# Kernel optimization log

Hardware: AMD Instinct MI355X
Metric: run time of the kernel (lower is better)

## Reference

```python
import jax, jax.numpy as jnp
import numpy as np

B, C, VC, H, W = 4, 256, 128, 64, 64


def setup_inputs() -> dict:
    key = jax.random.key(0)
    kx, kq, kk, kv = jax.random.split(key, 4)
    # Conv2d 1x1 no-bias weights are just [out_channels, in_channels] matrices.
    s = 1.0 / np.sqrt(C)
    return {
        "x": jax.random.normal(kx, (B, C, H, W), dtype=jnp.float32),
        "Wq": jax.random.uniform(kq, (VC, C), minval=-s, maxval=s, dtype=jnp.float32),
        "Wk": jax.random.uniform(kk, (VC, C), minval=-s, maxval=s, dtype=jnp.float32),
        "Wv": jax.random.uniform(kv, (VC, C), minval=-s, maxval=s, dtype=jnp.float32),
    }


def reference(x, Wq, Wk, Wv):
    # 1x1 convs == per-pixel channel GEMMs
    Q = jnp.einsum('bchw,dc->bdhw', x, Wq)  # [B, VC, H, W]
    K = jnp.einsum('bchw,dc->bdhw', x, Wk)
    V = jnp.einsum('bchw,dc->bdhw', x, Wv)
    b, d, h, w = Q.shape
    # affinity over all spatial pairs: [B, H, W, H, W]
    aff = jnp.einsum('bdij,bdkl->bijkl', Q, K).reshape(b, h, w, h * w)
    aff = jax.nn.softmax(aff, axis=3).reshape(b, h, w, h, w)
    # attention-weighted aggregation of values
    out = jnp.einsum('bijkl,bdkl->bdij', aff, V)  # [B, VC, H, W]
    return out
```

## Files before the change

### kernel.cpp

```cpp
#include <hip/hip_runtime.h>
#include <hip/hip_bf16.h>

#define B_ 4
#define C_ 256
#define D_ 128
#define N_ 4096

typedef float f32x4 __attribute__((ext_vector_type(4)));
typedef short bf16x8 __attribute__((ext_vector_type(8)));
typedef short s16x4 __attribute__((ext_vector_type(4)));
typedef unsigned short u16;
typedef unsigned int u32;

__device__ __forceinline__ u16 f2bf(float f) {
  unsigned u = __float_as_uint(f);
  u += 0x7fffu + ((u >> 16) & 1u);
  return (u16)(u >> 16);
}
__device__ __forceinline__ float bf2f(u16 v) {
  return __uint_as_float(((u32)v) << 16);
}
__device__ __forceinline__ u32 cvt_pk_bf16(float a, float b) {
  u32 r;
  asm("v_cvt_pk_bf16_f32 %0, %1, %2" : "=v"(r) : "v"(a), "v"(b));
  return r;
}

__global__ __launch_bounds__(256) void castw_kernel(
    const float* __restrict__ Wq, const float* __restrict__ Wk,
    const float* __restrict__ Wv, u16* __restrict__ Whi,
    u16* __restrict__ Wlo) {
  const int i = blockIdx.x * 256 + threadIdx.x;
  const int m = i >> 13;
  const int j = (i & 8191) * 4;
  const float* src = (m == 0) ? Wq : (m == 1) ? Wk : Wv;
  const float scale = (m == 0) ? 1.44269504f : 1.0f;
  const float4 v = *(const float4*)(src + j);
  const float vv[4] = {v.x * scale, v.y * scale, v.z * scale, v.w * scale};
  s16x4 h, l;
#pragma unroll
  for (int k = 0; k < 4; ++k) {
    const u16 hb = f2bf(vv[k]);
    h[k] = (short)hb;
    l[k] = (short)f2bf(vv[k] - bf2f(hb));
  }
  *(s16x4*)&Whi[m * 32768 + j] = h;
  *(s16x4*)&Wlo[m * 32768 + j] = l;
}

__global__ __launch_bounds__(256, 3) void proj_kernel(
    const float* __restrict__ x, const u16* __restrict__ Whi,
    const u16* __restrict__ Wlo, u16* __restrict__ Qo, u16* __restrict__ Ko,
    u16* __restrict__ Vt) {
  __shared__ __align__(16) u16 xs_h[32 * 256];
  __shared__ __align__(16) u16 xs_l[32 * 256];

  const int n0 = blockIdx.x * 32;
  const int b = blockIdx.y;
  const int z = blockIdx.z;
  const int t = threadIdx.x;
  const int w = t >> 6, lane = t & 63, g = lane >> 4, c = lane & 15;

  {
    const float* xb = x + ((size_t)b * C_) * N_ + n0;
#pragma unroll
    for (int r = 0; r < 8; ++r) {
      const int id = r * 256 + t;
      const int cr = id >> 3, nq = (id & 7) * 4;
      const float4 v = *(const float4*)(xb + (size_t)cr * N_ + nq);
      const float vv[4] = {v.x, v.y, v.z, v.w};
#pragma unroll
      for (int k2 = 0; k2 < 4; ++k2) {
        const int idx2 = (nq + k2) * 256 + (cr ^ (((nq + k2) & 7) << 3));
        const u16 hb = f2bf(vv[k2]);
        xs_h[idx2] = hb;
        xs_l[idx2] = f2bf(vv[k2] - bf2f(hb));
      }
    }
  }
  __syncthreads();

  if (w < 2) {
    const size_t wo = (size_t)w * 32768;
    u16* __restrict__ O = (w == 0 ? Qo : Ko) + (size_t)b * N_ * D_;
#pragma unroll 1
    for (int dti = 0; dti < 4; ++dti) {
      const int dt = z * 4 + dti;
      f32x4 a0 = {0.f, 0.f, 0.f, 0.f};
      f32x4 a1 = {0.f, 0.f, 0.f, 0.f};
#pragma unroll 1
      for (int kcb = 0; kcb < 2; ++kcb) {
        bf16x8 wfh[4], wfl[4];
#pragma unroll
        for (int j = 0; j < 4; ++j) {
          const size_t off = wo + (size_t)(dt * 16 + c) * 256 +
                             (kcb * 4 + j) * 32 + g * 8;
          wfh[j] = *(const bf16x8*)&Whi[off];
          wfl[j] = *(const bf16x8*)&Wlo[off];
        }
#pragma unroll
        for (int j = 0; j < 4; ++j) {
          const int kc = kcb * 4 + j;
          const int col = (kc * 32 + g * 8) ^ ((c & 7) << 3);
          const bf16x8 xh0 = *(const bf16x8*)&xs_h[c * 256 + col];
          const bf16x8 xl0 = *(const bf16x8*)&xs_l[c * 256 + col];
          const bf16x8 xh1 = *(const bf16x8*)&xs_h[(16 + c) * 256 + col];
          const bf16x8 xl1 = *(const bf16x8*)&xs_l[(16 + c) * 256 + col];
          a0 = __builtin_amdgcn_mfma_f32_16x16x32_bf16(xh0, wfh[j], a0, 0, 0, 0);
          a0 = __builtin_amdgcn_mfma_f32_16x16x32_bf16(xh0, wfl[j], a0, 0, 0, 0);
          a0 = __builtin_amdgcn_mfma_f32_16x16x32_bf16(xl0, wfh[j], a0, 0, 0, 0);
          a1 = __builtin_amdgcn_mfma_f32_16x16x32_bf16(xh1, wfh[j], a1, 0, 0, 0);
          a1 = __builtin_amdgcn_mfma_f32_16x16x32_bf16(xh1, wfl[j], a1, 0, 0, 0);
          a1 = __builtin_amdgcn_mfma_f32_16x16x32_bf16(xl1, wfh[j], a1, 0, 0, 0);
        }
      }
#pragma unroll
      for (int i = 0; i < 4; ++i) {
        O[(size_t)(n0 + g * 4 + i) * D_ + dt * 16 + c] = f2bf(a0[i]);
        O[(size_t)(n0 + 16 + g * 4 + i) * D_ + dt * 16 + c] = f2bf(a1[i]);
      }
    }
  } else {
    const size_t wo = (size_t)2 * 32768;
    const int d0 = (w - 2) * 64 + z * 32;
    u16* __restrict__ O = Vt + (size_t)b * D_ * N_;
#pragma unroll 1
    for (int dti = 0; dti < 2; ++dti) {
      const int dr = d0 + dti * 16;
      f32x4 a0 = {0.f, 0.f, 0.f, 0.f};
      f32x4 a1 = {0.f, 0.f, 0.f, 0.f};
#pragma unroll 1
      for (int kcb = 0; kcb < 2; ++kcb) {
        bf16x8 wfh[4], wfl[4];
#pragma unroll
        for (int j = 0; j < 4; ++j) {
          const size_t off =
              wo + (size_t)(dr + c) * 256 + (kcb * 4 + j) * 32 + g * 8;
          wfh[j] = *(const bf16x8*)&Whi[off];
          wfl[j] = *(const bf16x8*)&Wlo[off];
        }
#pragma unroll
        for (int j = 0; j < 4; ++j) {
          const int kc = kcb * 4 + j;
          const int col = (kc * 32 + g * 8) ^ ((c & 7) << 3);
          const bf16x8 xh0 = *(const bf16x8*)&xs_h[c * 256 + col];
          const bf16x8 xl0 = *(const bf16x8*)&xs_l[c * 256 + col];
          const bf16x8 xh1 = *(const bf16x8*)&xs_h[(16 + c) * 256 + col];
          const bf16x8 xl1 = *(const bf16x8*)&xs_l[(16 + c) * 256 + col];
          a0 = __builtin_amdgcn_mfma_f32_16x16x32_bf16(wfh[j], xh0, a0, 0, 0, 0);
          a0 = __builtin_amdgcn_mfma_f32_16x16x32_bf16(wfl[j], xh0, a0, 0, 0, 0);
          a0 = __builtin_amdgcn_mfma_f32_16x16x32_bf16(wfh[j], xl0, a0, 0, 0, 0);
          a1 = __builtin_amdgcn_mfma_f32_16x16x32_bf16(wfh[j], xh1, a1, 0, 0, 0);
          a1 = __builtin_amdgcn_mfma_f32_16x16x32_bf16(wfl[j], xh1, a1, 0, 0, 0);
          a1 = __builtin_amdgcn_mfma_f32_16x16x32_bf16(wfh[j], xl1, a1, 0, 0, 0);
        }
      }
#pragma unroll
      for (int i = 0; i < 4; ++i) {
        O[(size_t)(dr + g * 4 + i) * N_ + n0 + c] = f2bf(a0[i]);
        O[(size_t)(dr + g * 4 + i) * N_ + n0 + 16 + c] = f2bf(a1[i]);
      }
    }
  }
}

__device__ __forceinline__ int kIdx(int row, int col) {
  return row * 128 + (col ^ ((row & 7) << 3));
}
__device__ __forceinline__ int vIdx(int d, int col) {
  return d * 64 + (col ^ ((d & 7) << 3));
}
__device__ __forceinline__ int kprm(int q) {
  const int ct = q >> 2, qq = q & 3;
  return ((ct >> 1) << 5) +
         (((qq >> 1) == (ct & 1)) ? (qq << 3) : (((qq ^ 2) << 3) + 4));
}

__global__ __launch_bounds__(256, 2) void attn_kernel(
    const u16* __restrict__ Q, const u16* __restrict__ K,
    const u16* __restrict__ Vt, u16* __restrict__ op,
    float* __restrict__ mb, float* __restrict__ lb,
    float* __restrict__ outf, int qt, int rem, int S) {
  __shared__ __align__(16) u16 lds_k[64 * 128];
  __shared__ __align__(16) u16 lds_vt[128 * 64];

  const int L = blockIdx.x;
  int qx, b, sid;
  if (((B_ * S) & 7) == 0) {
    const int gpx = (B_ * S) >> 3;
    const int xcd = L & 7, idx = L >> 3;
    const int grp = xcd * gpx + (idx >> 5);
    qx = idx & 31;
    b = grp / S;
    sid = grp - b * S;
  } else {
    qx = L & 31;
    const int r2 = L >> 5;
    b = r2 % B_;
    sid = r2 / B_;
  }
  const int q0 = qx * 128;
  const int NT = qt + (sid < rem ? 1 : 0);
  const int t0 = sid * qt + (sid < rem ? sid : rem);
  const int k0 = t0 * 64;
  const int t = threadIdx.x;
  const int w = t >> 6, lane = t & 63, g = lane >> 4, c = lane & 15;
  const int qw = q0 + w * 32;
  const bool ghi = (g & 2) != 0;

  const u16* __restrict__ Qb = Q + (size_t)b * N_ * D_;
  const u16* __restrict__ Kb = K + (size_t)b * N_ * D_;
  const u16* __restrict__ Vb = Vt + (size_t)b * D_ * N_;

  bf16x8 qf[2][4];
#pragma unroll
  for (int qh = 0; qh < 2; ++qh)
#pragma unroll
    for (int kc = 0; kc < 4; ++kc)
      qf[qh][kc] =
          *(const bf16x8*)&Qb[(size_t)(qw + qh * 16 + c) * D_ + kc * 32 + g * 8];

  f32x4 acc[8][2];
  f32x4 accl[2];
#pragma unroll
  for (int dt = 0; dt < 8; ++dt)
#pragma unroll
    for (int qh = 0; qh < 2; ++qh) acc[dt][qh] = (f32x4){0.f, 0.f, 0.f, 0.f};
  accl[0] = (f32x4){0.f, 0.f, 0.f, 0.f};
  accl[1] = (f32x4){0.f, 0.f, 0.f, 0.f};
  float mrow[2] = {-3.0e38f, -3.0e38f};
  const float THR = 11.5415603f;

  bf16x8 onesv;
#pragma unroll
  for (int j = 0; j < 8; ++j) onesv[j] = (short)0x3F80;

  bf16x8 krg[4], vrg[4];
  auto load_tile = [&](int kbase) {
#pragma unroll
    for (int i = 0; i < 4; ++i) {
      const int idx = i * 256 + t;
      krg[i] = *(const bf16x8*)&Kb[(size_t)(kbase + (idx >> 4)) * D_ + (idx & 15) * 8];
      vrg[i] = *(const bf16x8*)&Vb[(size_t)(idx >> 3) * N_ + kbase + (idx & 7) * 8];
    }
  };
  load_tile(k0);

  for (int kt = 0; kt < NT; ++kt) {
    __syncthreads();
#pragma unroll
    for (int i = 0; i < 4; ++i) {
      const int idx = i * 256 + t;
      *(bf16x8*)&lds_k[kIdx(idx >> 4, (idx & 15) * 8)] = krg[i];
      const int d = idx >> 3, rc = idx & 7;
      s16x4 lo, hi;
      lo[0] = vrg[i][0]; lo[1] = vrg[i][1]; lo[2] = vrg[i][2]; lo[3] = vrg[i][3];
      hi[0] = vrg[i][4]; hi[1] = vrg[i][5]; hi[2] = vrg[i][6]; hi[3] = vrg[i][7];
      *(s16x4*)&lds_vt[vIdx(d, kprm(rc * 2))] = lo;
      *(s16x4*)&lds_vt[vIdx(d, kprm(rc * 2 + 1))] = hi;
    }
    if (kt + 1 < NT) load_tile(k0 + (kt + 1) * 64);
    __syncthreads();

    f32x4 s[4][2];
#pragma unroll
    for (int ct = 0; ct < 4; ++ct)
#pragma unroll
      for (int qh = 0; qh < 2; ++qh) s[ct][qh] = (f32x4){0.f, 0.f, 0.f, 0.f};
    __builtin_amdgcn_s_setprio(1);
#pragma unroll
    for (int kc = 0; kc < 4; ++kc) {
#pragma unroll
      for (int ct = 0; ct < 4; ++ct) {
        const bf16x8 kf =
            *(const bf16x8*)&lds_k[kIdx(ct * 16 + c, kc * 32 + g * 8)];
        s[ct][0] = __builtin_amdgcn_mfma_f32_16x16x32_bf16(kf, qf[0][kc], s[ct][0], 0, 0, 0);
        s[ct][1] = __builtin_amdgcn_mfma_f32_16x16x32_bf16(kf, qf[1][kc], s[ct][1], 0, 0, 0);
      }
    }
    __builtin_amdgcn_s_setprio(0);

    float pml[2];
#pragma unroll
    for (int qh = 0; qh < 2; ++qh) {
      const float m0 = fmaxf(fmaxf(s[0][qh][0], s[0][qh][1]),
                             fmaxf(s[0][qh][2], s[0][qh][3]));
      const float m1 = fmaxf(fmaxf(s[1][qh][0], s[1][qh][1]),
                             fmaxf(s[1][qh][2], s[1][qh][3]));
      const float m2 = fmaxf(fmaxf(s[2][qh][0], s[2][qh][1]),
                             fmaxf(s[2][qh][2], s[2][qh][3]));
      const float m3 = fmaxf(fmaxf(s[3][qh][0], s[3][qh][1]),
                             fmaxf(s[3][qh][2], s[3][qh][3]));
      pml[qh] = fmaxf(fmaxf(m0, m1), fmaxf(m2, m3));
    }
    const bool need =
        __any((pml[0] > mrow[0] + THR) || (pml[1] > mrow[1] + THR));
    if (need) {
#pragma unroll
      for (int qh = 0; qh < 2; ++qh) {
        float p = pml[qh];
        p = fmaxf(p, __shfl_xor(p, 16));
        p = fmaxf(p, __shfl_xor(p, 32));
        const float mnew = fmaxf(mrow[qh], p);
        const float scl = exp2f(mrow[qh] - mnew);
        mrow[qh] = mnew;
        accl[qh][0] *= scl; accl[qh][1] *= scl;
        accl[qh][2] *= scl; accl[qh][3] *= scl;
#pragma unroll
        for (int dt = 0; dt < 8; ++dt) {
          acc[dt][qh][0] *= scl; acc[dt][qh][1] *= scl;
          acc[dt][qh][2] *= scl; acc[dt][qh][3] *= scl;
        }
      }
    }
#pragma unroll
    for (int qh = 0; qh < 2; ++qh)
#pragma unroll
      for (int ct = 0; ct < 4; ++ct)
#pragma unroll
        for (int i = 0; i < 4; ++i)
          s[ct][qh][i] = exp2f(s[ct][qh][i] - mrow[qh]);

    u32 pfw[2][2][4];
#pragma unroll
    for (int kc = 0; kc < 2; ++kc) {
#pragma unroll
      for (int qh = 0; qh < 2; ++qh) {
        const u32 lo0 = cvt_pk_bf16(s[kc * 2][qh][0], s[kc * 2][qh][1]);
        const u32 lo1 = cvt_pk_bf16(s[kc * 2][qh][2], s[kc * 2][qh][3]);
        const u32 hi0 = cvt_pk_bf16(s[kc * 2 + 1][qh][0], s[kc * 2 + 1][qh][1]);
        const u32 hi1 = cvt_pk_bf16(s[kc * 2 + 1][qh][2], s[kc * 2 + 1][qh][3]);
        pfw[kc][qh][0] = ghi ? hi0 : lo0;
        pfw[kc][qh][1] = ghi ? hi1 : lo1;
        const u32 s0 = ghi ? lo0 : hi0;
        const u32 s1 = ghi ? lo1 : hi1;
        pfw[kc][qh][2] = (u32)__shfl_xor((int)s0, 32);
        pfw[kc][qh][3] = (u32)__shfl_xor((int)s1, 32);
      }
    }

#pragma unroll
    for (int kc = 0; kc < 2; ++kc) {
      union { u32 w[4]; bf16x8 v; } u0, u1;
#pragma unroll
      for (int j = 0; j < 4; ++j) { u0.w[j] = pfw[kc][0][j]; u1.w[j] = pfw[kc][1][j]; }
      __builtin_amdgcn_s_setprio(1);
      accl[0] = __builtin_amdgcn_mfma_f32_16x16x32_bf16(onesv, u0.v, accl[0], 0, 0, 0);
      accl[1] = __builtin_amdgcn_mfma_f32_16x16x32_bf16(onesv, u1.v, accl[1], 0, 0, 0);
#pragma unroll
      for (int dt = 0; dt < 8; ++dt) {
        const bf16x8 vf =
            *(const bf16x8*)&lds_vt[vIdx(dt * 16 + c, kc * 32 + g * 8)];
        acc[dt][0] = __builtin_amdgcn_mfma_f32_16x16x32_bf16(vf, u0.v, acc[dt][0], 0, 0, 0);
        acc[dt][1] = __builtin_amdgcn_mfma_f32_16x16x32_bf16(vf, u1.v, acc[dt][1], 0, 0, 0);
      }
      __builtin_amdgcn_s_setprio(0);
    }
  }

#pragma unroll
  for (int qh = 0; qh < 2; ++qh) {
    const int n = qw + qh * 16 + c;
    const float lr = accl[qh][0];
    if (mb) {
      u16* __restrict__ ob = op + ((size_t)(sid * B_ + b) * D_) * N_;
#pragma unroll
      for (int dt = 0; dt < 8; ++dt)
#pragma unroll
        for (int i = 0; i < 4; ++i)
          ob[(size_t)(dt * 16 + g * 4 + i) * N_ + n] = f2bf(acc[dt][qh][i]);
      if (g == 0) {
        mb[(size_t)(sid * B_ + b) * N_ + n] = mrow[qh];
        lb[(size_t)(sid * B_ + b) * N_ + n] = lr;
      }
    } else {
      const float linv = 1.0f / lr;
      float* __restrict__ ob = outf + (size_t)b * D_ * N_;
#pragma unroll
      for (int dt = 0; dt < 8; ++dt)
#pragma unroll
        for (int i = 0; i < 4; ++i)
          ob[(size_t)(dt * 16 + g * 4 + i) * N_ + n] = acc[dt][qh][i] * linv;
    }
  }
}

__global__ __launch_bounds__(256) void combine_kernel(
    const u16* __restrict__ op, const float* __restrict__ mbu,
    const float* __restrict__ lbu, float* __restrict__ out, int S) {
  const int idx = blockIdx.x * 256 + threadIdx.x;
  const int n0 = (idx & (N_ / 4 - 1)) * 4;
  const int bd = idx >> 10;
  const int b = bd >> 7, d = bd & (D_ - 1);

  float4 msv[8], lsv[8];
  float M0 = -3e38f, M1 = -3e38f, M2 = -3e38f, M3 = -3e38f;
#pragma unroll
  for (int s = 0; s < 8; ++s)
    if (s < S) {
      msv[s] = *(const float4*)&mbu[(size_t)(s * B_ + b) * N_ + n0];
      lsv[s] = *(const float4*)&lbu[(size_t)(s * B_ + b) * N_ + n0];
      M0 = fmaxf(M0, msv[s].x); M1 = fmaxf(M1, msv[s].y);
      M2 = fmaxf(M2, msv[s].z); M3 = fmaxf(M3, msv[s].w);
    }
  float d0 = 0.f, d1 = 0.f, d2 = 0.f, d3 = 0.f;
  float a0 = 0.f, a1 = 0.f, a2 = 0.f, a3 = 0.f;
#pragma unroll
  for (int s = 0; s < 8; ++s)
    if (s < S) {
      const float w0 = exp2f(msv[s].x - M0);
      const float w1 = exp2f(msv[s].y - M1);
      const float w2 = exp2f(msv[s].z - M2);
      const float w3 = exp2f(msv[s].w - M3);
      d0 += lsv[s].x * w0; d1 += lsv[s].y * w1;
      d2 += lsv[s].z * w2; d3 += lsv[s].w * w3;
      const s16x4 o =
          *(const s16x4*)&op[((size_t)(s * B_ + b) * D_ + d) * N_ + n0];
      a0 += w0 * bf2f((u16)o[0]); a1 += w1 * bf2f((u16)o[1]);
      a2 += w2 * bf2f((u16)o[2]); a3 += w3 * bf2f((u16)o[3]);
    }
  float4 r = {a0 / d0, a1 / d1, a2 / d2, a3 / d3};
  *(float4*)&out[((size_t)b * D_ + d) * N_ + n0] = r;
}

extern "C" void kernel_launch(void* const* d_in, const int* in_sizes, int n_in,
                              void* d_out, int out_size, void* d_ws, size_t ws_size,
                              hipStream_t stream) {
  const float* x  = (const float*)d_in[0];
  const float* Wq = (const float*)d_in[1];
  const float* Wk = (const float*)d_in[2];
  const float* Wv = (const float*)d_in[3];
  float* out = (float*)d_out;

  u16* whi  = (u16*)d_ws;
  u16* wlo  = whi + (size_t)3 * 128 * 256;
  u16* q_ws = wlo + (size_t)3 * 128 * 256;
  u16* k_ws = q_ws + (size_t)B_ * N_ * D_;
  u16* v_ws = k_ws + (size_t)B_ * N_ * D_;

  castw_kernel<<<96, 256, 0, stream>>>(Wq, Wk, Wv, whi, wlo);
  proj_kernel<<<dim3(N_ / 32, B_, 2), 256, 0, stream>>>(x, whi, wlo, q_ws,
                                                        k_ws, v_ws);

  const size_t baseB =
      ((size_t)6 * 128 * 256 + (size_t)3 * B_ * N_ * D_) * 2;
  int S = 0;
  const int cands[4] = {6, 4, 2, 1};
  for (int ci = 0; ci < 4; ++ci) {
    const int cand = cands[ci];
    const size_t need = baseB + (size_t)cand * ((size_t)B_ * D_ * N_ * 2 +
                                                (size_t)2 * B_ * N_ * 4);
    if (ws_size >= need) { S = cand; break; }
  }
  if (S > 1) {
    u16* opb = (u16*)((char*)d_ws + baseB);
    float* mbuf = (float*)(opb + (size_t)S * B_ * D_ * N_);
    float* lbuf = mbuf + (size_t)S * B_ * N_;
    attn_kernel<<<dim3(32 * B_ * S), 256, 0, stream>>>(
        q_ws, k_ws, v_ws, opb, mbuf, lbuf, nullptr, 64 / S, 64 % S, S);
    combine_kernel<<<(B_ * D_ * N_ / 4) / 256, 256, 0, stream>>>(opb, mbuf,
                                                                 lbuf, out, S);
  } else {
    attn_kernel<<<dim3(32 * B_), 256, 0, stream>>>(
        q_ws, k_ws, v_ws, nullptr, nullptr, nullptr, out, 64, 0, 1);
  }
}
```

Baseline: 101.6 us.

## Halve attention query tile per block to raise occupancy and drop split count

```diff
diff --git a/kernel.cpp b/kernel.cpp
--- a/kernel.cpp
+++ b/kernel.cpp
@@ -176,7 +176,7 @@
          (((qq >> 1) == (ct & 1)) ? (qq << 3) : (((qq ^ 2) << 3) + 4));
 }
 
-__global__ __launch_bounds__(256, 2) void attn_kernel(
+__global__ __launch_bounds__(256, 4) void attn_kernel(
     const u16* __restrict__ Q, const u16* __restrict__ K,
     const u16* __restrict__ Vt, u16* __restrict__ op,
     float* __restrict__ mb, float* __restrict__ lb,
@@ -189,46 +189,40 @@
   if (((B_ * S) & 7) == 0) {
     const int gpx = (B_ * S) >> 3;
     const int xcd = L & 7, idx = L >> 3;
-    const int grp = xcd * gpx + (idx >> 5);
-    qx = idx & 31;
+    const int grp = xcd * gpx + (idx >> 6);
+    qx = idx & 63;
     b = grp / S;
     sid = grp - b * S;
   } else {
-    qx = L & 31;
-    const int r2 = L >> 5;
+    qx = L & 63;
+    const int r2 = L >> 6;
     b = r2 % B_;
     sid = r2 / B_;
   }
-  const int q0 = qx * 128;
+  const int q0 = qx * 64;
   const int NT = qt + (sid < rem ? 1 : 0);
   const int t0 = sid * qt + (sid < rem ? sid : rem);
   const int k0 = t0 * 64;
   const int t = threadIdx.x;
   const int w = t >> 6, lane = t & 63, g = lane >> 4, c = lane & 15;
-  const int qw = q0 + w * 32;
+  const int qw = q0 + w * 16;
   const bool ghi = (g & 2) != 0;
 
   const u16* __restrict__ Qb = Q + (size_t)b * N_ * D_;
   const u16* __restrict__ Kb = K + (size_t)b * N_ * D_;
   const u16* __restrict__ Vb = Vt + (size_t)b * D_ * N_;
 
-  bf16x8 qf[2][4];
-#pragma unroll
-  for (int qh = 0; qh < 2; ++qh)
-#pragma unroll
-    for (int kc = 0; kc < 4; ++kc)
-      qf[qh][kc] =
-          *(const bf16x8*)&Qb[(size_t)(qw + qh * 16 + c) * D_ + kc * 32 + g * 8];
-
-  f32x4 acc[8][2];
-  f32x4 accl[2];
-#pragma unroll
-  for (int dt = 0; dt < 8; ++dt)
-#pragma unroll
-    for (int qh = 0; qh < 2; ++qh) acc[dt][qh] = (f32x4){0.f, 0.f, 0.f, 0.f};
-  accl[0] = (f32x4){0.f, 0.f, 0.f, 0.f};
-  accl[1] = (f32x4){0.f, 0.f, 0.f, 0.f};
-  float mrow[2] = {-3.0e38f, -3.0e38f};
+  bf16x8 qf[4];
+#pragma unroll
+  for (int kc = 0; kc < 4; ++kc)
+    qf[kc] = *(const bf16x8*)&Qb[(size_t)(qw + c) * D_ + kc * 32 + g * 8];
+
+  f32x4 acc[8];
+  f32x4 accl;
+#pragma unroll
+  for (int dt = 0; dt < 8; ++dt) acc[dt] = (f32x4){0.f, 0.f, 0.f, 0.f};
+  accl = (f32x4){0.f, 0.f, 0.f, 0.f};
+  float mrow = -3.0e38f;
   const float THR = 11.5415603f;
 
   bf16x8 onesv;
@@ -262,11 +256,9 @@
     if (kt + 1 < NT) load_tile(k0 + (kt + 1) * 64);
     __syncthreads();
 
-    f32x4 s[4][2];
-#pragma unroll
-    for (int ct = 0; ct < 4; ++ct)
-#pragma unroll
-      for (int qh = 0; qh < 2; ++qh) s[ct][qh] = (f32x4){0.f, 0.f, 0.f, 0.f};
+    f32x4 s[4];
+#pragma unroll
+    for (int ct = 0; ct < 4; ++ct) s[ct] = (f32x4){0.f, 0.f, 0.f, 0.f};
     __builtin_amdgcn_s_setprio(1);
 #pragma unroll
     for (int kc = 0; kc < 4; ++kc) {
@@ -274,103 +266,83 @@
       for (int ct = 0; ct < 4; ++ct) {
         const bf16x8 kf =
             *(const bf16x8*)&lds_k[kIdx(ct * 16 + c, kc * 32 + g * 8)];
-        s[ct][0] = __builtin_amdgcn_mfma_f32_16x16x32_bf16(kf, qf[0][kc], s[ct][0], 0, 0, 0);
-        s[ct][1] = __builtin_amdgcn_mfma_f32_16x16x32_bf16(kf, qf[1][kc], s[ct][1], 0, 0, 0);
+        s[ct] = __builtin_amdgcn_mfma_f32_16x16x32_bf16(kf, qf[kc], s[ct], 0, 0, 0);
       }
     }
     __builtin_amdgcn_s_setprio(0);
 
-    float pml[2];
-#pragma unroll
-    for (int qh = 0; qh < 2; ++qh) {
-      const float m0 = fmaxf(fmaxf(s[0][qh][0], s[0][qh][1]),
-                             fmaxf(s[0][qh][2], s[0][qh][3]));
-      const float m1 = fmaxf(fmaxf(s[1][qh][0], s[1][qh][1]),
-                             fmaxf(s[1][qh][2], s[1][qh][3]));
-      const float m2 = fmaxf(fmaxf(s[2][qh][0], s[2][qh][1]),
-                             fmaxf(s[2][qh][2], s[2][qh][3]));
-      const float m3 = fmaxf(fmaxf(s[3][qh][0], s[3][qh][1]),
-                             fmaxf(s[3][qh][2], s[3][qh][3]));
-      pml[qh] = fmaxf(fmaxf(m0, m1), fmaxf(m2, m3));
-    }
-    const bool need =
-        __any((pml[0] > mrow[0] + THR) || (pml[1] > mrow[1] + THR));
+    float pml;
+    {
+      const float m0 = fmaxf(fmaxf(s[0][0], s[0][1]), fmaxf(s[0][2], s[0][3]));
+      const float m1 = fmaxf(fmaxf(s[1][0], s[1][1]), fmaxf(s[1][2], s[1][3]));
+      const float m2 = fmaxf(fmaxf(s[2][0], s[2][1]), fmaxf(s[2][2], s[2][3]));
+      const float m3 = fmaxf(fmaxf(s[3][0], s[3][1]), fmaxf(s[3][2], s[3][3]));
+      pml = fmaxf(fmaxf(m0, m1), fmaxf(m2, m3));
+    }
+    const bool need = __any(pml > mrow + THR);
     if (need) {
-#pragma unroll
-      for (int qh = 0; qh < 2; ++qh) {
-        float p = pml[qh];
-        p = fmaxf(p, __shfl_xor(p, 16));
-        p = fmaxf(p, __shfl_xor(p, 32));
-        const float mnew = fmaxf(mrow[qh], p);
-        const float scl = exp2f(mrow[qh] - mnew);
-        mrow[qh] = mnew;
-        accl[qh][0] *= scl; accl[qh][1] *= scl;
-        accl[qh][2] *= scl; accl[qh][3] *= scl;
-#pragma unroll
-        for (int dt = 0; dt < 8; ++dt) {
-          acc[dt][qh][0] *= scl; acc[dt][qh][1] *= scl;
-          acc[dt][qh][2] *= scl; acc[dt][qh][3] *= scl;
-        }
-      }
-    }
-#pragma unroll
-    for (int qh = 0; qh < 2; ++qh)
-#pragma unroll
-      for (int ct = 0; ct < 4; ++ct)
-#pragma unroll
-        for (int i = 0; i < 4; ++i)
-          s[ct][qh][i] = exp2f(s[ct][qh][i] - mrow[qh]);
-
-    u32 pfw[2][2][4];
+      float p = pml;
+      p = fmaxf(p, __shfl_xor(p, 16));
+      p = fmaxf(p, __shfl_xor(p, 32));
+      const float mnew = fmaxf(mrow, p);
+      const float scl = exp2f(mrow - mnew);
+      mrow = mnew;
+      accl[0] *= scl; accl[1] *= scl; accl[2] *= scl; accl[3] *= scl;
+#pragma unroll
+      for (int dt = 0; dt < 8; ++dt) {
+        acc[dt][0] *= scl; acc[dt][1] *= scl;
+        acc[dt][2] *= scl; acc[dt][3] *= scl;
+      }
+    }
+#pragma unroll
+    for (int ct = 0; ct < 4; ++ct)
+#pragma unroll
+      for (int i = 0; i < 4; ++i) s[ct][i] = exp2f(s[ct][i] - mrow);
+
+    u32 pfw[2][4];
 #pragma unroll
     for (int kc = 0; kc < 2; ++kc) {
-#pragma unroll
-      for (int qh = 0; qh < 2; ++qh) {
-        const u32 lo0 = cvt_pk_bf16(s[kc * 2][qh][0], s[kc * 2][qh][1]);
-        const u32 lo1 = cvt_pk_bf16(s[kc * 2][qh][2], s[kc * 2][qh][3]);
-        const u32 hi0 = cvt_pk_bf16(s[kc * 2 + 1][qh][0], s[kc * 2 + 1][qh][1]);
-        const u32 hi1 = cvt_pk_bf16(s[kc * 2 + 1][qh][2], s[kc * 2 + 1][qh][3]);
-        pfw[kc][qh][0] = ghi ? hi0 : lo0;
-        pfw[kc][qh][1] = ghi ? hi1 : lo1;
-        const u32 s0 = ghi ? lo0 : hi0;
-        const u32 s1 = ghi ? lo1 : hi1;
-        pfw[kc][qh][2] = (u32)__shfl_xor((int)s0, 32);
-        pfw[kc][qh][3] = (u32)__shfl_xor((int)s1, 32);
-      }
+      const u32 lo0 = cvt_pk_bf16(s[kc * 2][0], s[kc * 2][1]);
+      const u32 lo1 = cvt_pk_bf16(s[kc * 2][2], s[kc * 2][3]);
+      const u32 hi0 = cvt_pk_bf16(s[kc * 2 + 1][0], s[kc * 2 + 1][1]);
+      const u32 hi1 = cvt_pk_bf16(s[kc * 2 + 1][2], s[kc * 2 + 1][3]);
+      pfw[kc][0] = ghi ? hi0 : lo0;
+      pfw[kc][1] = ghi ? hi1 : lo1;
+      const u32 s0 = ghi ? lo0 : hi0;
+      const u32 s1 = ghi ? lo1 : hi1;
+      pfw[kc][2] = (u32)__shfl_xor((int)s0, 32);
+      pfw[kc][3] = (u32)__shfl_xor((int)s1, 32);
     }
 
 #pragma unroll
     for (int kc = 0; kc < 2; ++kc) {
-      union { u32 w[4]; bf16x8 v; } u0, u1;
-#pragma unroll
-      for (int j = 0; j < 4; ++j) { u0.w[j] = pfw[kc][0][j]; u1.w[j] = pfw[kc][1][j]; }
+      union { u32 w[4]; bf16x8 v; } u0;
+#pragma unroll
+      for (int j = 0; j < 4; ++j) u0.w[j] = pfw[kc][j];
       __builtin_amdgcn_s_setprio(1);
-      accl[0] = __builtin_amdgcn_mfma_f32_16x16x32_bf16(onesv, u0.v, accl[0], 0, 0, 0);
-      accl[1] = __builtin_amdgcn_mfma_f32_16x16x32_bf16(onesv, u1.v, accl[1], 0, 0, 0);
+      accl = __builtin_amdgcn_mfma_f32_16x16x32_bf16(onesv, u0.v, accl, 0, 0, 0);
 #pragma unroll
       for (int dt = 0; dt < 8; ++dt) {
         const bf16x8 vf =
             *(const bf16x8*)&lds_vt[vIdx(dt * 16 + c, kc * 32 + g * 8)];
-        acc[dt][0] = __builtin_amdgcn_mfma_f32_16x16x32_bf16(vf, u0.v, acc[dt][0], 0, 0, 0);
-        acc[dt][1] = __builtin_amdgcn_mfma_f32_16x16x32_bf16(vf, u1.v, acc[dt][1], 0, 0, 0);
+        acc[dt] = __builtin_amdgcn_mfma_f32_16x16x32_bf16(vf, u0.v, acc[dt], 0, 0, 0);
       }
       __builtin_amdgcn_s_setprio(0);
     }
   }
 
-#pragma unroll
-  for (int qh = 0; qh < 2; ++qh) {
-    const int n = qw + qh * 16 + c;
-    const float lr = accl[qh][0];
+  {
+    const int n = qw + c;
+    const float lr = accl[0];
     if (mb) {
       u16* __restrict__ ob = op + ((size_t)(sid * B_ + b) * D_) * N_;
 #pragma unroll
       for (int dt = 0; dt < 8; ++dt)
 #pragma unroll
         for (int i = 0; i < 4; ++i)
-          ob[(size_t)(dt * 16 + g * 4 + i) * N_ + n] = f2bf(acc[dt][qh][i]);
+          ob[(size_t)(dt * 16 + g * 4 + i) * N_ + n] = f2bf(acc[dt][i]);
       if (g == 0) {
-        mb[(size_t)(sid * B_ + b) * N_ + n] = mrow[qh];
+        mb[(size_t)(sid * B_ + b) * N_ + n] = mrow;
         lb[(size_t)(sid * B_ + b) * N_ + n] = lr;
       }
     } else {
@@ -380,7 +352,7 @@
       for (int dt = 0; dt < 8; ++dt)
 #pragma unroll
         for (int i = 0; i < 4; ++i)
-          ob[(size_t)(dt * 16 + g * 4 + i) * N_ + n] = acc[dt][qh][i] * linv;
+          ob[(size_t)(dt * 16 + g * 4 + i) * N_ + n] = acc[dt][i] * linv;
     }
   }
 }
@@ -445,8 +417,8 @@
   const size_t baseB =
       ((size_t)6 * 128 * 256 + (size_t)3 * B_ * N_ * D_) * 2;
   int S = 0;
-  const int cands[4] = {6, 4, 2, 1};
-  for (int ci = 0; ci < 4; ++ci) {
+  const int cands[3] = {4, 2, 1};
+  for (int ci = 0; ci < 3; ++ci) {
     const int cand = cands[ci];
     const size_t need = baseB + (size_t)cand * ((size_t)B_ * D_ * N_ * 2 +
                                                 (size_t)2 * B_ * N_ * 4);
@@ -456,12 +428,12 @@
     u16* opb = (u16*)((char*)d_ws + baseB);
     float* mbuf = (float*)(opb + (size_t)S * B_ * D_ * N_);
     float* lbuf = mbuf + (size_t)S * B_ * N_;
-    attn_kernel<<<dim3(32 * B_ * S), 256, 0, stream>>>(
+    attn_kernel<<<dim3(64 * B_ * S), 256, 0, stream>>>(
         q_ws, k_ws, v_ws, opb, mbuf, lbuf, nullptr, 64 / S, 64 % S, S);
     combine_kernel<<<(B_ * D_ * N_ / 4) / 256, 256, 0, stream>>>(opb, mbuf,
                                                                  lbuf, out, S);
   } else {
-    attn_kernel<<<dim3(32 * B_), 256, 0, stream>>>(
+    attn_kernel<<<dim3(64 * B_), 256, 0, stream>>>(
         q_ws, k_ws, v_ws, nullptr, nullptr, nullptr, out, 64, 0, 1);
   }
 }
```

New measurement: 129.2 us. 1.27x slower.

## Process two K/V tiles per barrier pair with doubled LDS staging

Applied to the files above, without the earlier changes.

```diff
diff --git a/kernel.cpp b/kernel.cpp
--- a/kernel.cpp
+++ b/kernel.cpp
@@ -181,8 +181,8 @@
     const u16* __restrict__ Vt, u16* __restrict__ op,
     float* __restrict__ mb, float* __restrict__ lb,
     float* __restrict__ outf, int qt, int rem, int S) {
-  __shared__ __align__(16) u16 lds_k[64 * 128];
-  __shared__ __align__(16) u16 lds_vt[128 * 64];
+  __shared__ __align__(16) u16 lds_k[2][64 * 128];
+  __shared__ __align__(16) u16 lds_vt[2][128 * 64];
 
   const int L = blockIdx.x;
   int qx, b, sid;
@@ -235,33 +235,23 @@
 #pragma unroll
   for (int j = 0; j < 8; ++j) onesv[j] = (short)0x3F80;
 
-  bf16x8 krg[4], vrg[4];
-  auto load_tile = [&](int kbase) {
-#pragma unroll
-    for (int i = 0; i < 4; ++i) {
-      const int idx = i * 256 + t;
-      krg[i] = *(const bf16x8*)&Kb[(size_t)(kbase + (idx >> 4)) * D_ + (idx & 15) * 8];
-      vrg[i] = *(const bf16x8*)&Vb[(size_t)(idx >> 3) * N_ + kbase + (idx & 7) * 8];
-    }
+  bf16x8 krg[8], vrg[8];
+  auto load_pair = [&](int kbase) {
+#pragma unroll
+    for (int h = 0; h < 2; ++h)
+#pragma unroll
+      for (int i = 0; i < 4; ++i) {
+        const int idx = i * 256 + t;
+        const int kb2 = kbase + h * 64;
+        krg[h * 4 + i] =
+            *(const bf16x8*)&Kb[(size_t)(kb2 + (idx >> 4)) * D_ + (idx & 15) * 8];
+        vrg[h * 4 + i] =
+            *(const bf16x8*)&Vb[(size_t)(idx >> 3) * N_ + kb2 + (idx & 7) * 8];
+      }
   };
-  load_tile(k0);
-
-  for (int kt = 0; kt < NT; ++kt) {
-    __syncthreads();
-#pragma unroll
-    for (int i = 0; i < 4; ++i) {
-      const int idx = i * 256 + t;
-      *(bf16x8*)&lds_k[kIdx(idx >> 4, (idx & 15) * 8)] = krg[i];
-      const int d = idx >> 3, rc = idx & 7;
-      s16x4 lo, hi;
-      lo[0] = vrg[i][0]; lo[1] = vrg[i][1]; lo[2] = vrg[i][2]; lo[3] = vrg[i][3];
-      hi[0] = vrg[i][4]; hi[1] = vrg[i][5]; hi[2] = vrg[i][6]; hi[3] = vrg[i][7];
-      *(s16x4*)&lds_vt[vIdx(d, kprm(rc * 2))] = lo;
-      *(s16x4*)&lds_vt[vIdx(d, kprm(rc * 2 + 1))] = hi;
-    }
-    if (kt + 1 < NT) load_tile(k0 + (kt + 1) * 64);
-    __syncthreads();
-
+  load_pair(k0);
+
+  auto proc = [&](const u16* kb, const u16* vb) {
     f32x4 s[4][2];
 #pragma unroll
     for (int ct = 0; ct < 4; ++ct)
@@ -272,8 +262,7 @@
     for (int kc = 0; kc < 4; ++kc) {
 #pragma unroll
       for (int ct = 0; ct < 4; ++ct) {
-        const bf16x8 kf =
-            *(const bf16x8*)&lds_k[kIdx(ct * 16 + c, kc * 32 + g * 8)];
+        const bf16x8 kf = *(const bf16x8*)&kb[kIdx(ct * 16 + c, kc * 32 + g * 8)];
         s[ct][0] = __builtin_amdgcn_mfma_f32_16x16x32_bf16(kf, qf[0][kc], s[ct][0], 0, 0, 0);
         s[ct][1] = __builtin_amdgcn_mfma_f32_16x16x32_bf16(kf, qf[1][kc], s[ct][1], 0, 0, 0);
       }
@@ -341,21 +330,43 @@
 
 #pragma unroll
     for (int kc = 0; kc < 2; ++kc) {
-      union { u32 w[4]; bf16x8 v; } u0, u1;
-#pragma unroll
-      for (int j = 0; j < 4; ++j) { u0.w[j] = pfw[kc][0][j]; u1.w[j] = pfw[kc][1][j]; }
+      union { u32 w2[4]; bf16x8 v; } u0, u1;
+#pragma unroll
+      for (int j = 0; j < 4; ++j) { u0.w2[j] = pfw[kc][0][j]; u1.w2[j] = pfw[kc][1][j]; }
       __builtin_amdgcn_s_setprio(1);
       accl[0] = __builtin_amdgcn_mfma_f32_16x16x32_bf16(onesv, u0.v, accl[0], 0, 0, 0);
       accl[1] = __builtin_amdgcn_mfma_f32_16x16x32_bf16(onesv, u1.v, accl[1], 0, 0, 0);
 #pragma unroll
       for (int dt = 0; dt < 8; ++dt) {
-        const bf16x8 vf =
-            *(const bf16x8*)&lds_vt[vIdx(dt * 16 + c, kc * 32 + g * 8)];
+        const bf16x8 vf = *(const bf16x8*)&vb[vIdx(dt * 16 + c, kc * 32 + g * 8)];
         acc[dt][0] = __builtin_amdgcn_mfma_f32_16x16x32_bf16(vf, u0.v, acc[dt][0], 0, 0, 0);
         acc[dt][1] = __builtin_amdgcn_mfma_f32_16x16x32_bf16(vf, u1.v, acc[dt][1], 0, 0, 0);
       }
       __builtin_amdgcn_s_setprio(0);
     }
+  };
+
+  for (int kt = 0; kt < NT; kt += 2) {
+    __syncthreads();
+#pragma unroll
+    for (int h = 0; h < 2; ++h)
+#pragma unroll
+      for (int i = 0; i < 4; ++i) {
+        const int idx = i * 256 + t;
+        *(bf16x8*)&lds_k[h][kIdx(idx >> 4, (idx & 15) * 8)] = krg[h * 4 + i];
+        const int d = idx >> 3, rc = idx & 7;
+        const bf16x8 vv = vrg[h * 4 + i];
+        s16x4 lo, hi;
+        lo[0] = vv[0]; lo[1] = vv[1]; lo[2] = vv[2]; lo[3] = vv[3];
+        hi[0] = vv[4]; hi[1] = vv[5]; hi[2] = vv[6]; hi[3] = vv[7];
+        *(s16x4*)&lds_vt[h][vIdx(d, kprm(rc * 2))] = lo;
+        *(s16x4*)&lds_vt[h][vIdx(d, kprm(rc * 2 + 1))] = hi;
+      }
+    if (kt + 2 < NT) load_pair(k0 + (kt + 2) * 64);
+    __syncthreads();
+
+    proc(&lds_k[0][0], &lds_vt[0][0]);
+    proc(&lds_k[1][0], &lds_vt[1][0]);
   }
 
 #pragma unroll
@@ -445,8 +456,8 @@
   const size_t baseB =
       ((size_t)6 * 128 * 256 + (size_t)3 * B_ * N_ * D_) * 2;
   int S = 0;
-  const int cands[4] = {6, 4, 2, 1};
-  for (int ci = 0; ci < 4; ++ci) {
+  const int cands[3] = {4, 2, 1};
+  for (int ci = 0; ci < 3; ++ci) {
     const int cand = cands[ci];
     const size_t need = baseB + (size_t)cand * ((size_t)B_ * D_ * N_ * 2 +
                                                 (size_t)2 * B_ * N_ * 4);
```

New measurement: 96.68 us. 4.9% less time.
